# Kernel optimization log

Hardware: AMD Instinct MI355X
Metric: run time of the kernel (lower is better)

## Reference

```python
import jax, jax.numpy as jnp
import numpy as np

H = 1024          # hidden_size
I = 4096          # intermediate_size
TAU = 9           # hashcode_len
LN_EPS = 1e-12    # layer_norm_eps


def setup_inputs() -> dict:
    key = jax.random.key(0)
    k1, k2, k3, k4 = jax.random.split(key, 4)
    return {
        "hidden_states": jax.random.normal(k1, (4, 2048, H), jnp.float32),
        "ln_weight": jnp.ones((H,), jnp.float32),
        "ln_bias": jnp.zeros((H,), jnp.float32),
        "k_weight": 0.02 * jax.random.normal(k2, (I, H), jnp.float32),
        "q_weight": 0.02 * jax.random.normal(k3, (I, H), jnp.float32),
        "bias": 0.001 * jax.random.normal(k4, (H,), jnp.float32),
    }


def _l2_normalize(x):
    # matches F.normalize(x, dim=-1): x / max(||x||, 1e-12)
    n = jnp.sqrt(jnp.sum(x * x, axis=-1, keepdims=True))
    return x / jnp.maximum(n, 1e-12)


def reference(hidden_states, ln_weight, ln_bias, k_weight, q_weight, bias):
    lead_shape = hidden_states.shape[:-1]
    x = hidden_states.reshape(-1, H)  # [N, H]

    # LayerNorm
    mu = jnp.mean(x, axis=-1, keepdims=True)
    var = jnp.mean(jnp.square(x - mu), axis=-1, keepdims=True)
    x = (x - mu) * jax.lax.rsqrt(var + LN_EPS) * ln_weight + ln_bias

    # YOSO expectation kernel: B_ij = (1 - arccos(<q_i, k_j>)/pi)^tau
    Q = _l2_normalize(x)         # [N, H]
    K = _l2_normalize(k_weight)  # [I, H]
    s = jnp.clip(jnp.einsum('nh,ih->ni', Q, K), -1.0 + 1e-6, 1.0 - 1e-6)
    B = jnp.power(1.0 - jnp.arccos(s) / jnp.pi, TAU)  # [N, I]

    X = jnp.einsum('ni,ih->nh', B, q_weight)  # V = q_weight
    X = _l2_normalize(X) + bias
    return X.reshape(*lead_shape, H)
```

## Files before the change

### kernel.cpp

```cpp
#include <hip/hip_runtime.h>

#define HD 1024
#define ID 4096
#define NR 8192

typedef float f32x4 __attribute__((ext_vector_type(4)));
typedef __bf16 bf16x8 __attribute__((ext_vector_type(8)));
typedef int i32x8 __attribute__((ext_vector_type(8)));

__device__ inline ushort f2bf(float f) {
    union { float f; unsigned u; } v; v.f = f;
    unsigned u = v.u;
    unsigned r = (u + 0x7fffu + ((u >> 16) & 1u)) >> 16;
    return (ushort)r;
}

__device__ inline float wave_sum(float v) {
#pragma unroll
    for (int o = 32; o > 0; o >>= 1) v += __shfl_xor(v, o, 64);
    return v;
}

__device__ __forceinline__ float yoso_act(float v) {
    float s = fminf(fmaxf(v, -0.999999f), 0.999999f);
    float a = fabsf(s);
    float p = 0.49998557f + a * (-0.06751706f + a * (0.02363794f - a * 0.00596170f));
    float q = sqrtf(1.0f - a) * p;
    float tt = (s >= 0.0f) ? 1.0f - q : q;
    float t2 = tt * tt, t4 = t2 * t2, t8 = t4 * t4;
    return t8 * tt;
}

__global__ __launch_bounds__(256, 3) void gemm1f_kernel(
    const unsigned char* __restrict__ Ap, const unsigned char* __restrict__ Bp,
    ushort* __restrict__ Cp, int N, int K) {
    __shared__ unsigned char la[128 * 128] __attribute__((aligned(16)));
    __shared__ unsigned char lb[128 * 128] __attribute__((aligned(16)));
    const int tid = threadIdx.x;
    const int w = tid >> 6, lane = tid & 63;
    const int bid = blockIdx.x;
    const int xcd = bid & 7, cu = (bid >> 3) & 31, rnd = bid >> 8;
    const int brow = (xcd * 8 + (cu >> 2)) * 128;
    const int bcol = (rnd * 4 + (cu & 3)) * 128;
    const int wr = (w >> 1) * 64;
    const int wc = (w & 1) * 64;
    f32x4 acc[4][4] = {};
    const int srow = lane >> 3;
    const int scolb = ((lane & 7) ^ (lane >> 3)) << 4;

    for (int k0 = 0; k0 < K; k0 += 128) {
#pragma unroll
        for (int it = 0; it < 4; ++it) {
            const int rb = w * 32 + it * 8;
            const unsigned char* ga = Ap + (size_t)(brow + rb + srow) * K + k0 + scolb;
            const unsigned char* gb = Bp + (size_t)(bcol + rb + srow) * K + k0 + scolb;
            __builtin_amdgcn_global_load_lds(
                (const __attribute__((address_space(1))) void*)ga,
                (__attribute__((address_space(3))) void*)&la[rb * 128], 16, 0, 0);
            __builtin_amdgcn_global_load_lds(
                (const __attribute__((address_space(1))) void*)gb,
                (__attribute__((address_space(3))) void*)&lb[rb * 128], 16, 0, 0);
        }
        __syncthreads();
        i32x8 af[4], bfr[4];
        const int base = (lane >> 4) << 5;
#pragma unroll
        for (int m = 0; m < 4; ++m) {
            const int row = wr + m * 16 + (lane & 15);
            const int key = (row & 7) << 4;
            const uint4 lo = *(const uint4*)(la + row * 128 + (base ^ key));
            const uint4 hi = *(const uint4*)(la + row * 128 + ((base + 16) ^ key));
            af[m] = (i32x8){(int)lo.x, (int)lo.y, (int)lo.z, (int)lo.w,
                            (int)hi.x, (int)hi.y, (int)hi.z, (int)hi.w};
        }
#pragma unroll
        for (int n = 0; n < 4; ++n) {
            const int row = wc + n * 16 + (lane & 15);
            const int key = (row & 7) << 4;
            const uint4 lo = *(const uint4*)(lb + row * 128 + (base ^ key));
            const uint4 hi = *(const uint4*)(lb + row * 128 + ((base + 16) ^ key));
            bfr[n] = (i32x8){(int)lo.x, (int)lo.y, (int)lo.z, (int)lo.w,
                             (int)hi.x, (int)hi.y, (int)hi.z, (int)hi.w};
        }
#pragma unroll
        for (int m = 0; m < 4; ++m)
#pragma unroll
            for (int n = 0; n < 4; ++n)
                acc[m][n] = __builtin_amdgcn_mfma_scale_f32_16x16x128_f8f6f4(
                    af[m], bfr[n], acc[m][n], 0, 0,
                    0, 0x7F7F7F7F, 0, 0x7F7F7F7F);
        __syncthreads();
    }
    const int crow0 = brow + wr + ((lane >> 4) << 2);
    const int ccol0 = bcol + wc + (lane & 15);
#pragma unroll
    for (int m = 0; m < 4; ++m)
#pragma unroll
        for (int n = 0; n < 4; ++n)
#pragma unroll
            for (int r = 0; r < 4; ++r) {
                int row = crow0 + m * 16 + r;
                int col = ccol0 + n * 16;
                Cp[(size_t)row * N + col] =
                    f2bf(yoso_act(acc[m][n][r] * 0.00390625f));
            }
}

__global__ __launch_bounds__(512) void gemm2k_kernel(
    const ushort* __restrict__ Ap, const ushort* __restrict__ Bp,
    float* __restrict__ Cv, int N, int K, int nt) {
    __shared__ char lds[98304] __attribute__((aligned(16)));
    const int tid = threadIdx.x;
    const int w = tid >> 6, lane = tid & 63;
    const int wm = w >> 1, wn = w & 1;
    const int bid = blockIdx.x;
    const int xcd = bid & 7, cu = bid >> 3;
    const int brow = (xcd * 4 + (cu >> 3)) * 256;
    const int bcol = (cu & 7) * 128;
    const int strow = tid >> 4;
    const int sslot = (tid & 15) ^ (strow & 15);
    const int scolb = sslot << 4;

    f32x4 acc[4][4] = {};

    auto stage = [&](int t) {
#pragma unroll
        for (int u = 0; u < 8; ++u) {
            int grow = brow + u * 32 + strow;
            const char* src = (const char*)Ap + ((size_t)grow * K + t * 128) * 2 + scolb;
            __builtin_amdgcn_global_load_lds(
                (const __attribute__((address_space(1))) void*)src,
                (__attribute__((address_space(3))) void*)&lds[u * 8192 + tid * 16], 16, 0, 0);
        }
#pragma unroll
        for (int u = 0; u < 4; ++u) {
            int grow = bcol + u * 32 + strow;
            const char* src = (const char*)Bp + ((size_t)grow * K + t * 128) * 2 + scolb;
            __builtin_amdgcn_global_load_lds(
                (const __attribute__((address_space(1))) void*)src,
                (__attribute__((address_space(3))) void*)&lds[65536 + u * 8192 + tid * 16],
                16, 0, 0);
        }
    };

    for (int t = 0; t < nt; ++t) {
        stage(t);
        __syncthreads();
#pragma unroll
        for (int ks = 0; ks < 4; ++ks) {
            bf16x8 af[4], bfr[4];
            const int ckey = lane & 15;
            const int chunk = ks * 4 + (lane >> 4);
#pragma unroll
            for (int m = 0; m < 4; ++m) {
                int row = wm * 64 + m * 16 + (lane & 15);
                af[m] = *(const bf16x8*)(lds + row * 256 + ((chunk ^ ckey) << 4));
            }
#pragma unroll
            for (int n = 0; n < 4; ++n) {
                int row = wn * 64 + n * 16 + (lane & 15);
                bfr[n] = *(const bf16x8*)(lds + 65536 + row * 256 + ((chunk ^ ckey) << 4));
            }
#pragma unroll
            for (int m = 0; m < 4; ++m)
#pragma unroll
                for (int n = 0; n < 4; ++n)
                    acc[m][n] = __builtin_amdgcn_mfma_f32_16x16x32_bf16(
                        af[m], bfr[n], acc[m][n], 0, 0, 0);
        }
        __syncthreads();
    }

    const int crow0 = brow + wm * 64 + ((lane >> 4) << 2);
    const int ccol0 = bcol + wn * 64 + (lane & 15);
#pragma unroll
    for (int m = 0; m < 4; ++m)
#pragma unroll
        for (int n = 0; n < 4; ++n)
#pragma unroll
            for (int r = 0; r < 4; ++r) {
                int row = crow0 + m * 16 + r;
                int col = ccol0 + n * 16;
                Cv[(size_t)row * N + col] = acc[m][n][r];
            }
}

__global__ __launch_bounds__(256) void prep_kernel(
    const float* __restrict__ hs, const float* __restrict__ lnw,
    const float* __restrict__ lnb, const float* __restrict__ kw,
    const float* __restrict__ qw, unsigned char* __restrict__ Qf,
    unsigned char* __restrict__ Kf, ushort* __restrict__ VT) {
    __shared__ float smem[64][65];
    const int b = blockIdx.x, t = threadIdx.x;
    const int lane = t & 63, wid = t >> 6;
    if (b < NR) {
        const float4 v = reinterpret_cast<const float4*>(hs + (size_t)b * HD)[t];
        float s  = v.x + v.y + v.z + v.w;
        float ss = v.x*v.x + v.y*v.y + v.z*v.z + v.w*v.w;
        s = wave_sum(s); ss = wave_sum(ss);
        if (lane == 0) { smem[0][wid] = s; smem[1][wid] = ss; }
        __syncthreads();
        float st  = smem[0][0] + smem[0][1] + smem[0][2] + smem[0][3];
        float sst = smem[1][0] + smem[1][1] + smem[1][2] + smem[1][3];
        float mu   = st * (1.0f / HD);
        float var  = sst * (1.0f / HD) - mu * mu;
        float rstd = rsqrtf(var + 1e-12f);
        const float4 wv = reinterpret_cast<const float4*>(lnw)[t];
        const float4 bv = reinterpret_cast<const float4*>(lnb)[t];
        float y0 = (v.x - mu) * rstd * wv.x + bv.x;
        float y1 = (v.y - mu) * rstd * wv.y + bv.y;
        float y2 = (v.z - mu) * rstd * wv.z + bv.z;
        float y3 = (v.w - mu) * rstd * wv.w + bv.w;
        float n2 = wave_sum(y0*y0 + y1*y1 + y2*y2 + y3*y3);
        if (lane == 0) smem[2][wid] = n2;
        __syncthreads();
        float nt2 = smem[2][0] + smem[2][1] + smem[2][2] + smem[2][3];
        float sc = 16.0f / fmaxf(sqrtf(nt2), 1e-12f);
        int r = __builtin_amdgcn_cvt_pk_fp8_f32(y0 * sc, y1 * sc, 0, false);
        r = __builtin_amdgcn_cvt_pk_fp8_f32(y2 * sc, y3 * sc, r, true);
        reinterpret_cast<int*>(Qf + (size_t)b * HD)[t] = r;
    } else if (b < NR + ID) {
        const int row = b - NR;
        const float4 v = reinterpret_cast<const float4*>(kw + (size_t)row * HD)[t];
        float n2 = wave_sum(v.x*v.x + v.y*v.y + v.z*v.z + v.w*v.w);
        if (lane == 0) smem[0][wid] = n2;
        __syncthreads();
        float nt2 = smem[0][0] + smem[0][1] + smem[0][2] + smem[0][3];
        float sc = 16.0f / fmaxf(sqrtf(nt2), 1e-12f);
        int r = __builtin_amdgcn_cvt_pk_fp8_f32(v.x * sc, v.y * sc, 0, false);
        r = __builtin_amdgcn_cvt_pk_fp8_f32(v.z * sc, v.w * sc, r, true);
        reinterpret_cast<int*>(Kf + (size_t)row * HD)[t] = r;
    } else {
        const int b2 = b - NR - ID;
        const int bi = (b2 & 63) * 64, bh = (b2 >> 6) * 64;
        const int r0 = t >> 4, c0 = (t & 15) << 2;
#pragma unroll
        for (int rr = 0; rr < 64; rr += 16) {
            float4 val = *reinterpret_cast<const float4*>(
                &qw[(size_t)(bi + rr + r0) * HD + bh + c0]);
            smem[rr + r0][c0 + 0] = val.x; smem[rr + r0][c0 + 1] = val.y;
            smem[rr + r0][c0 + 2] = val.z; smem[rr + r0][c0 + 3] = val.w;
        }
        __syncthreads();
#pragma unroll
        for (int rr = 0; rr < 64; rr += 16) {
            ushort4 o;
            o.x = f2bf(smem[c0 + 0][rr + r0]);
            o.y = f2bf(smem[c0 + 1][rr + r0]);
            o.z = f2bf(smem[c0 + 2][rr + r0]);
            o.w = f2bf(smem[c0 + 3][rr + r0]);
            *reinterpret_cast<ushort4*>(&VT[(size_t)(bh + rr + r0) * ID + bi + c0]) = o;
        }
    }
}

__global__ __launch_bounds__(256) void outnorm_kernel(
    float* __restrict__ X, const float* __restrict__ bias) {
    __shared__ float red2[4];
    const int row = blockIdx.x, t = threadIdx.x;
    const int lane = t & 63, wid = t >> 6;
    float4 v = reinterpret_cast<float4*>(X + (size_t)row * HD)[t];
    float n2 = wave_sum(v.x*v.x + v.y*v.y + v.z*v.z + v.w*v.w);
    if (lane == 0) red2[wid] = n2;
    __syncthreads();
    float nt = red2[0] + red2[1] + red2[2] + red2[3];
    float sc = 1.0f / fmaxf(sqrtf(nt), 1e-12f);
    const float4 bv = reinterpret_cast<const float4*>(bias)[t];
    float4 o;
    o.x = v.x * sc + bv.x; o.y = v.y * sc + bv.y;
    o.z = v.z * sc + bv.z; o.w = v.w * sc + bv.w;
    reinterpret_cast<float4*>(X + (size_t)row * HD)[t] = o;
}

extern "C" void kernel_launch(void* const* d_in, const int* in_sizes, int n_in,
                              void* d_out, int out_size, void* d_ws, size_t ws_size,
                              hipStream_t stream) {
    const float* hs   = (const float*)d_in[0];
    const float* lnw  = (const float*)d_in[1];
    const float* lnb  = (const float*)d_in[2];
    const float* kw   = (const float*)d_in[3];
    const float* qw   = (const float*)d_in[4];
    const float* bias = (const float*)d_in[5];
    float* out = (float*)d_out;

    char* ws = (char*)d_ws;
    unsigned char* Qf = (unsigned char*)(ws);
    unsigned char* Kf = (unsigned char*)(ws + (size_t)8388608);
    ushort* VT   = (ushort*)(ws + (size_t)12582912);
    ushort* Bmat = (ushort*)(ws + (size_t)20971520);

    prep_kernel<<<NR + ID + 1024, 256, 0, stream>>>(hs, lnw, lnb, kw, qw, Qf, Kf, VT);
    gemm1f_kernel<<<(NR / 128) * (ID / 128), 256, 0, stream>>>(
        Qf, Kf, Bmat, ID, HD);
    gemm2k_kernel<<<(NR / 256) * (HD / 128), 512, 0, stream>>>(
        Bmat, VT, out, HD, ID, ID / 128);
    outnorm_kernel<<<NR, 256, 0, stream>>>(out, bias);
}
```

Measured before the change: 167.2 us.

## Double-buffer LDS in second GEMM with halved K tile

```diff
diff --git a/kernel.cpp b/kernel.cpp
--- a/kernel.cpp
+++ b/kernel.cpp
@@ -106,7 +106,7 @@
             }
 }
 
-__global__ __launch_bounds__(512) void gemm2k_kernel(
+__global__ __launch_bounds__(512) void gemm2d_kernel(
     const ushort* __restrict__ Ap, const ushort* __restrict__ Bp,
     float* __restrict__ Cv, int N, int K, int nt) {
     __shared__ char lds[98304] __attribute__((aligned(16)));
@@ -117,49 +117,55 @@
     const int xcd = bid & 7, cu = bid >> 3;
     const int brow = (xcd * 4 + (cu >> 3)) * 256;
     const int bcol = (cu & 7) * 128;
-    const int strow = tid >> 4;
-    const int sslot = (tid & 15) ^ (strow & 15);
-    const int scolb = sslot << 4;
+    const int srow = lane >> 3;
+    const int scolb = ((lane & 7) ^ (lane >> 3)) << 4;
 
     f32x4 acc[4][4] = {};
 
-    auto stage = [&](int t) {
-#pragma unroll
-        for (int u = 0; u < 8; ++u) {
-            int grow = brow + u * 32 + strow;
-            const char* src = (const char*)Ap + ((size_t)grow * K + t * 128) * 2 + scolb;
+    auto stage = [&](int t, int db) {
+#pragma unroll
+        for (int u = 0; u < 4; ++u) {
+            int grow = brow + u * 64 + w * 8 + srow;
+            const char* src = (const char*)Ap + ((size_t)grow * K + t * 64) * 2 + scolb;
             __builtin_amdgcn_global_load_lds(
                 (const __attribute__((address_space(1))) void*)src,
-                (__attribute__((address_space(3))) void*)&lds[u * 8192 + tid * 16], 16, 0, 0);
-        }
-#pragma unroll
-        for (int u = 0; u < 4; ++u) {
-            int grow = bcol + u * 32 + strow;
-            const char* src = (const char*)Bp + ((size_t)grow * K + t * 128) * 2 + scolb;
+                (__attribute__((address_space(3))) void*)&lds[db * 32768 + u * 8192 + w * 1024],
+                16, 0, 0);
+        }
+#pragma unroll
+        for (int u = 0; u < 2; ++u) {
+            int grow = bcol + u * 64 + w * 8 + srow;
+            const char* src = (const char*)Bp + ((size_t)grow * K + t * 64) * 2 + scolb;
             __builtin_amdgcn_global_load_lds(
                 (const __attribute__((address_space(1))) void*)src,
-                (__attribute__((address_space(3))) void*)&lds[65536 + u * 8192 + tid * 16],
+                (__attribute__((address_space(3))) void*)&lds[65536 + db * 16384 + u * 8192 + w * 1024],
                 16, 0, 0);
         }
     };
 
+    stage(0, 0);
+    asm volatile("s_waitcnt vmcnt(0)" ::: "memory");
+    __builtin_amdgcn_s_barrier();
+
     for (int t = 0; t < nt; ++t) {
-        stage(t);
-        __syncthreads();
-#pragma unroll
-        for (int ks = 0; ks < 4; ++ks) {
+        const int db = t & 1;
+        const bool more = (t + 1 < nt);
+        if (more) stage(t + 1, db ^ 1);
+#pragma unroll
+        for (int ks = 0; ks < 2; ++ks) {
             bf16x8 af[4], bfr[4];
-            const int ckey = lane & 15;
             const int chunk = ks * 4 + (lane >> 4);
 #pragma unroll
             for (int m = 0; m < 4; ++m) {
                 int row = wm * 64 + m * 16 + (lane & 15);
-                af[m] = *(const bf16x8*)(lds + row * 256 + ((chunk ^ ckey) << 4));
+                af[m] = *(const bf16x8*)(lds + db * 32768 + row * 128 +
+                                         ((chunk ^ (row & 7)) << 4));
             }
 #pragma unroll
             for (int n = 0; n < 4; ++n) {
                 int row = wn * 64 + n * 16 + (lane & 15);
-                bfr[n] = *(const bf16x8*)(lds + 65536 + row * 256 + ((chunk ^ ckey) << 4));
+                bfr[n] = *(const bf16x8*)(lds + 65536 + db * 16384 + row * 128 +
+                                          ((chunk ^ (row & 7)) << 4));
             }
 #pragma unroll
             for (int m = 0; m < 4; ++m)
@@ -168,7 +174,11 @@
                     acc[m][n] = __builtin_amdgcn_mfma_f32_16x16x32_bf16(
                         af[m], bfr[n], acc[m][n], 0, 0, 0);
         }
-        __syncthreads();
+        if (more) {
+            __builtin_amdgcn_sched_barrier(0);
+            asm volatile("s_waitcnt vmcnt(0)" ::: "memory");
+            __builtin_amdgcn_s_barrier();
+        }
     }
 
     const int crow0 = brow + wm * 64 + ((lane >> 4) << 2);
@@ -292,7 +302,7 @@
     prep_kernel<<<NR + ID + 1024, 256, 0, stream>>>(hs, lnw, lnb, kw, qw, Qf, Kf, VT);
     gemm1f_kernel<<<(NR / 128) * (ID / 128), 256, 0, stream>>>(
         Qf, Kf, Bmat, ID, HD);
-    gemm2k_kernel<<<(NR / 256) * (HD / 128), 512, 0, stream>>>(
-        Bmat, VT, out, HD, ID, ID / 128);
+    gemm2d_kernel<<<(NR / 256) * (HD / 128), 512, 0, stream>>>(
+        Bmat, VT, out, HD, ID, ID / 64);
     outnorm_kernel<<<NR, 256, 0, stream>>>(out, bias);
 }
```

Measured after the change: 154.1 us. 7.9% less time.
